# Optimization experiments

Hardware: AMD Instinct MI355X
Metric: run time of the kernel (lower is better)

## Reference

```python
import jax, jax.numpy as jnp
import numpy as np

L = 5          # num_layers
N = 50000      # nodes
E = 600000     # edges
D = 128        # num_features == hidden_units
G = 256        # graphs in batch
O = 10         # num_outputs
BN_EPS = 1e-5


def setup_inputs() -> dict:
    key = jax.random.key(0)
    ks = jax.random.split(key, 8)
    x = jax.random.normal(ks[0], (N, D), jnp.float32)
    edge_index = jax.random.randint(ks[1], (2, E), 0, N, jnp.int32)
    edge_attr = jax.random.randint(ks[2], (E, 3), 0, 8, jnp.int32)
    batch = jnp.sort(jax.random.randint(ks[3], (N,), 0, G, jnp.int32))
    s = 0.05
    return {
        "x": x,
        "edge_index": edge_index,
        "edge_attr": edge_attr,
        "batch": batch,
        "bond_emb": jax.random.normal(ks[4], (L, 3, 8, D), jnp.float32) * s,
        "conv_w1": jax.random.normal(ks[5], (L, D, D), jnp.float32) * s,
        "conv_b1": jnp.zeros((L, D), jnp.float32),
        "conv_bn_gamma": jnp.ones((L, D), jnp.float32),
        "conv_bn_beta": jnp.zeros((L, D), jnp.float32),
        "conv_bn_mean": jnp.zeros((L, D), jnp.float32),
        "conv_bn_var": jnp.ones((L, D), jnp.float32),
        "conv_w2": jax.random.normal(ks[6], (L, D, D), jnp.float32) * s,
        "conv_b2": jnp.zeros((L, D), jnp.float32),
        "bn_gamma": jnp.ones((L, D), jnp.float32),
        "bn_beta": jnp.zeros((L, D), jnp.float32),
        "bn_mean": jnp.zeros((L, D), jnp.float32),
        "bn_var": jnp.ones((L, D), jnp.float32),
        "fc_w": jax.random.normal(ks[7], (L + 1, D, O), jnp.float32) * s,
        "fc_b": jnp.zeros((L + 1, O), jnp.float32),
    }


def _bn_eval(h, gamma, beta, mean, var):
    return (h - mean) * jax.lax.rsqrt(var + BN_EPS) * gamma + beta


def reference(x, edge_index, edge_attr, batch, bond_emb,
              conv_w1, conv_b1, conv_bn_gamma, conv_bn_beta, conv_bn_mean, conv_bn_var,
              conv_w2, conv_b2, bn_gamma, bn_beta, bn_mean, bn_var, fc_w, fc_b):
    src, dst = edge_index[0], edge_index[1]  # x_j = x[src], aggregate at dst
    feat_ids = jnp.arange(3)
    outs = [x]
    for i in range(L):
        # BondEncoder: sum of per-feature embeddings -> [E, D]
        ea = bond_emb[i][feat_ids, edge_attr].sum(axis=1)
        # GINEConv (eps=0): msg = relu(x_j + edge_attr), scatter-add, nn(x + aggr)
        msg = jax.nn.relu(x[src] + ea)
        aggr = jax.ops.segment_sum(msg, dst, num_segments=N)
        h = x + aggr
        h = h @ conv_w1[i] + conv_b1[i]
        h = jax.nn.relu(_bn_eval(h, conv_bn_gamma[i], conv_bn_beta[i], conv_bn_mean[i], conv_bn_var[i]))
        h = h @ conv_w2[i] + conv_b2[i]
        x = jax.nn.relu(_bn_eval(h, bn_gamma[i], bn_beta[i], bn_mean[i], bn_var[i]))
        outs.append(x)
    # global mean pool per layer output, linear head, sum (dropout = identity in eval)
    counts = jax.ops.segment_sum(jnp.ones((N,), x.dtype), batch, num_segments=G)
    inv = 1.0 / jnp.maximum(counts, 1.0)
    out = jnp.zeros((G, O), x.dtype)
    for i, h in enumerate(outs):
        pooled = jax.ops.segment_sum(h, batch, num_segments=G) * inv[:, None]
        out = out + pooled @ fc_w[i] + fc_b[i]
    return out
```

## Files before the change

### kernel.cpp

```cpp
#include <hip/hip_runtime.h>

#define NN 50000
#define EE 600000
#define DD 128
#define GG 256
#define LL 5
#define OO 10
#define BN_EPS 1e-5f
#define CPAD 513
#define ESTRIDE 40
#define SENT (512u << 16)

#define B_SCAT  2344
#define B_CVT   3125
#define B_COMBO 1283
#define B_WT    160
#define B_INV   1
#define B_POOL0 391
#define B_STREAM (B_CVT + B_COMBO + B_WT + B_INV + B_POOL0)
#define B_PREP  (B_SCAT + B_STREAM)

typedef __attribute__((ext_vector_type(8))) short short8;
typedef __attribute__((ext_vector_type(16))) float float16;

__device__ __forceinline__ unsigned short f2b(float f) {
    unsigned u = __float_as_uint(f);
    unsigned r = u + 0x7FFFu + ((u >> 16) & 1u);
    return (unsigned short)(r >> 16);
}
__device__ __forceinline__ unsigned pk2(float lo, float hi) {
    return (unsigned)f2b(lo) | ((unsigned)f2b(hi) << 16);
}
__device__ __forceinline__ float blo(unsigned u) { return __uint_as_float(u << 16); }
__device__ __forceinline__ float bhi(unsigned u) { return __uint_as_float(u & 0xFFFF0000u); }

__launch_bounds__(256)
__global__ void prep(const float* __restrict__ x, const int* __restrict__ ei,
                     const int* __restrict__ eattr, const int* __restrict__ batch,
                     const float* __restrict__ bond,
                     const float* __restrict__ w1, const float* __restrict__ w2,
                     unsigned* __restrict__ xb4, unsigned short* __restrict__ combo,
                     short* __restrict__ wt, int* __restrict__ epos,
                     unsigned* __restrict__ e_info,
                     float* __restrict__ inv, float* __restrict__ pooled0) {
    const int bid = blockIdx.x, t = threadIdx.x;
    const int sc = (bid % 3 == 0) ? (bid / 3) : B_SCAT;
    if (sc < B_SCAT) {
        int e = sc * 256 + t;
        if (e < EE) {
            int dst = ei[EE + e];
            int slot = atomicAdd(&epos[dst], 1);
            if (slot < ESTRIDE) {
                unsigned cidx = (unsigned)eattr[e * 3 + 0] | ((unsigned)eattr[e * 3 + 1] << 3)
                              | ((unsigned)eattr[e * 3 + 2] << 6);
                e_info[dst * ESTRIDE + slot] = (unsigned)ei[e] | (cidx << 16);
            }
        }
        return;
    }
    int pr = (bid + 2) / 3; if (pr > B_SCAT) pr = B_SCAT;
    const int ob = bid - pr;
    if (ob < B_CVT) {
        int gid = ob * 256 + t;
        const float4* xp = (const float4*)(x + (size_t)gid * 8);
        float4 a = xp[0], b = xp[1];
        uint4 o;
        o.x = pk2(a.x, a.y); o.y = pk2(a.z, a.w);
        o.z = pk2(b.x, b.y); o.w = pk2(b.z, b.w);
        ((uint4*)xb4)[gid] = o;
    } else if (ob < B_CVT + B_COMBO) {
        int e = (ob - B_CVT) * 256 + t;
        if (e < LL * CPAD * DD) {
            int l = e / (CPAD * DD), rem = e - l * (CPAD * DD);
            int c = rem / DD, d = rem - c * DD;
            float s;
            if (c == 512) s = -1e30f;
            else {
                const float* b_ = bond + (size_t)l * 3 * 8 * DD;
                s = b_[(c & 7) * DD + d] + b_[(8 + ((c >> 3) & 7)) * DD + d]
                  + b_[(16 + (c >> 6)) * DD + d];
            }
            combo[e] = f2b(s);
        }
    } else if (ob < B_CVT + B_COMBO + B_WT) {
        __shared__ float tile[32][33];
        int b = ob - B_CVT - B_COMBO;
        int mat = b >> 4, tl = b & 15;
        int k0 = (tl >> 2) * 32, c0 = (tl & 3) * 32;
        const float* W = (mat < 5) ? (w1 + (size_t)mat * DD * DD)
                                   : (w2 + (size_t)(mat - 5) * DD * DD);
        int j = t & 31, q = t >> 5;
#pragma unroll
        for (int rr = 0; rr < 4; ++rr) {
            int row = q + rr * 8;
            tile[row][j] = W[(size_t)(k0 + row) * DD + c0 + j];
        }
        __syncthreads();
#pragma unroll
        for (int rr = 0; rr < 4; ++rr) {
            int cr = q + rr * 8;
            wt[(size_t)mat * DD * DD + (size_t)(c0 + cr) * DD + k0 + j] = (short)f2b(tile[j][cr]);
        }
    } else if (ob < B_CVT + B_COMBO + B_WT + B_INV) {
        __shared__ int sg[GG + 1];
        int g = t, lo = 0, hi = NN;
        while (lo < hi) { int m = (lo + hi) >> 1; if (batch[m] < g) lo = m + 1; else hi = m; }
        sg[g] = lo;
        if (g == 0) sg[GG] = NN;
        __syncthreads();
        inv[g] = 1.0f / fmaxf((float)(sg[g + 1] - sg[g]), 1.0f);
    } else {
        int b = ob - (B_CVT + B_COMBO + B_WT + B_INV);
        int n0 = b * 128;
        __shared__ int sb[128];
        __shared__ float part[4][DD];
        if (t < 128) { int row = n0 + t; sb[t] = (row < NN) ? batch[row] : -1; }
        ((float*)part)[t] = 0.f;
        ((float*)part)[t + 256] = 0.f;
        __syncthreads();
        int gmin = sb[0];
        int col = t & 127, rh = t >> 7;
        float pg[4] = {0.f, 0.f, 0.f, 0.f};
        for (int r = rh; r < 128; r += 2) {
            int s = sb[r];
            float v = (s >= 0) ? x[(size_t)(n0 + r) * DD + col] : 0.f;
            int dg = s - gmin;
#pragma unroll
            for (int jj = 0; jj < 4; ++jj) pg[jj] += (dg == jj) ? v : 0.f;
        }
#pragma unroll
        for (int jj = 0; jj < 4; ++jj)
            if (pg[jj] != 0.f) atomicAdd(&part[jj][col], pg[jj]);
        __syncthreads();
        for (int q2 = t; q2 < 4 * DD; q2 += 256) {
            int jj = q2 >> 7, c2 = q2 & 127;
            float v = part[jj][c2];
            if (v != 0.f && gmin + jj < GG) atomicAdd(&pooled0[(gmin + jj) * DD + c2], v);
        }
    }
}

__launch_bounds__(256)
__global__ void aggr_csr(const unsigned short* __restrict__ xin,
                         const int* __restrict__ epos,
                         const unsigned* __restrict__ e_info,
                         const unsigned short* __restrict__ combo,
                         unsigned short* __restrict__ hin) {
    int node = blockIdx.x * 4 + (threadIdx.x >> 6);
    int lane = threadIdx.x & 63;
    if (node >= NN) return;
    const int base = node * ESTRIDE;
    int deg = epos[node]; if (deg > ESTRIDE) deg = ESTRIDE;
    const int dend = base + deg;
    const int pe   = base + ((deg + 7) & ~7);
    const int eg   = lane >> 4;
    const int f    = (lane & 15) * 8;
    float acc[8];
#pragma unroll
    for (int i = 0; i < 8; ++i) acc[i] = 0.f;

    for (int p = base; p < pe; p += 8) {
        unsigned i0 = e_info[p + eg];
        unsigned i1 = e_info[p + 4 + eg];
        if (p + eg >= dend)     i0 = SENT;
        if (p + 4 + eg >= dend) i1 = SENT;
        uint4 xv0 = *(const uint4*)&xin[(size_t)(i0 & 0xFFFFu) * DD + f];
        uint4 cv0 = *(const uint4*)&combo[(size_t)(i0 >> 16) * DD + f];
        uint4 xv1 = *(const uint4*)&xin[(size_t)(i1 & 0xFFFFu) * DD + f];
        uint4 cv1 = *(const uint4*)&combo[(size_t)(i1 >> 16) * DD + f];
        acc[0] += fmaxf(blo(xv0.x) + blo(cv0.x), 0.f) + fmaxf(blo(xv1.x) + blo(cv1.x), 0.f);
        acc[1] += fmaxf(bhi(xv0.x) + bhi(cv0.x), 0.f) + fmaxf(bhi(xv1.x) + bhi(cv1.x), 0.f);
        acc[2] += fmaxf(blo(xv0.y) + blo(cv0.y), 0.f) + fmaxf(blo(xv1.y) + blo(cv1.y), 0.f);
        acc[3] += fmaxf(bhi(xv0.y) + bhi(cv0.y), 0.f) + fmaxf(bhi(xv1.y) + bhi(cv1.y), 0.f);
        acc[4] += fmaxf(blo(xv0.z) + blo(cv0.z), 0.f) + fmaxf(blo(xv1.z) + blo(cv1.z), 0.f);
        acc[5] += fmaxf(bhi(xv0.z) + bhi(cv0.z), 0.f) + fmaxf(bhi(xv1.z) + bhi(cv1.z), 0.f);
        acc[6] += fmaxf(blo(xv0.w) + blo(cv0.w), 0.f) + fmaxf(blo(xv1.w) + blo(cv1.w), 0.f);
        acc[7] += fmaxf(bhi(xv0.w) + bhi(cv0.w), 0.f) + fmaxf(bhi(xv1.w) + bhi(cv1.w), 0.f);
    }
#pragma unroll
    for (int i = 0; i < 8; ++i) {
        acc[i] += __shfl_xor(acc[i], 16, 64);
        acc[i] += __shfl_xor(acc[i], 32, 64);
    }
    if (lane < 16) {
        uint4 self = *(const uint4*)&xin[(size_t)node * DD + f];
        uint4 o;
        o.x = pk2(acc[0] + blo(self.x), acc[1] + bhi(self.x));
        o.y = pk2(acc[2] + blo(self.y), acc[3] + bhi(self.y));
        o.z = pk2(acc[4] + blo(self.z), acc[5] + bhi(self.z));
        o.w = pk2(acc[6] + blo(self.w), acc[7] + bhi(self.w));
        *(uint4*)&hin[(size_t)node * DD + f] = o;
    }
}

__launch_bounds__(256)
__global__ void conv_fused(const unsigned short* __restrict__ hin,
                           const short* __restrict__ Wt1, const short* __restrict__ Wt2,
                           const float* __restrict__ b1, const float* __restrict__ g1,
                           const float* __restrict__ be1, const float* __restrict__ m1,
                           const float* __restrict__ v1,
                           const float* __restrict__ b2, const float* __restrict__ g2,
                           const float* __restrict__ be2, const float* __restrict__ m2,
                           const float* __restrict__ v2,
                           const int* __restrict__ batch,
                           unsigned short* __restrict__ outb,
                           float* __restrict__ pool_slot) {
    __shared__ short As[64 * 136];
    __shared__ int sbg[64];
    const int tid  = threadIdx.x;
    const int lane = tid & 63;
    const int wave = tid >> 6;
    const int row0 = blockIdx.x * 64;

    const int col   = wave * 32 + (lane & 31);
    const int khalf = (lane >> 5) * 8;
    const int arow  = lane & 31;
    const int rbase = 4 * (lane >> 5);
    const int gmin  = batch[row0];

    short8 bf[8];
#pragma unroll
    for (int ch = 0; ch < 8; ++ch)
        bf[ch] = *(const short8*)&Wt1[col * DD + ch * 16 + khalf];

    const float sc1 = g1[col] * rsqrtf(v1[col] + BN_EPS);
    const float sh1 = fmaf(b1[col] - m1[col], sc1, be1[col]);
    const float sc2 = g2[col] * rsqrtf(v2[col] + BN_EPS);
    const float sh2 = fmaf(b2[col] - m2[col], sc2, be2[col]);

    if (tid < 64) {
        int row = row0 + tid;
        sbg[tid] = (row < NN) ? batch[row] - gmin : -1;
    }
    for (int i = tid; i < 1024; i += 256) {
        int r = i >> 4, c8 = (i & 15) * 8;
        int row = row0 + r;
        uint4 z = make_uint4(0, 0, 0, 0);
        if (row < NN) z = *(const uint4*)&hin[(size_t)row * DD + c8];
        *(uint4*)&As[r * 136 + c8] = z;
    }
    __syncthreads();

    float16 acc0 = {0.f,0.f,0.f,0.f,0.f,0.f,0.f,0.f,0.f,0.f,0.f,0.f,0.f,0.f,0.f,0.f};
    float16 acc1 = acc0;
#pragma unroll
    for (int ch = 0; ch < 8; ++ch) {
        short8 a0 = *(const short8*)&As[(arow     ) * 136 + ch * 16 + khalf];
        short8 a1 = *(const short8*)&As[(32 + arow) * 136 + ch * 16 + khalf];
        acc0 = __builtin_amdgcn_mfma_f32_32x32x16_bf16(a0, bf[ch], acc0, 0, 0, 0);
        acc1 = __builtin_amdgcn_mfma_f32_32x32x16_bf16(a1, bf[ch], acc1, 0, 0, 0);
    }

#pragma unroll
    for (int ch = 0; ch < 8; ++ch)
        bf[ch] = *(const short8*)&Wt2[col * DD + ch * 16 + khalf];

    __syncthreads();
#pragma unroll
    for (int r = 0; r < 16; ++r) {
        int rl = (r & 3) + 8 * (r >> 2) + rbase;
        As[rl * 136 + col]        = (short)f2b(fmaxf(fmaf(acc0[r], sc1, sh1), 0.f));
        As[(32 + rl) * 136 + col] = (short)f2b(fmaxf(fmaf(acc1[r], sc1, sh1), 0.f));
    }
    __syncthreads();

    acc0 = acc1 = float16{0.f,0.f,0.f,0.f,0.f,0.f,0.f,0.f,0.f,0.f,0.f,0.f,0.f,0.f,0.f,0.f};
#pragma unroll
    for (int ch = 0; ch < 8; ++ch) {
        short8 a0 = *(const short8*)&As[(arow     ) * 136 + ch * 16 + khalf];
        short8 a1 = *(const short8*)&As[(32 + arow) * 136 + ch * 16 + khalf];
        acc0 = __builtin_amdgcn_mfma_f32_32x32x16_bf16(a0, bf[ch], acc0, 0, 0, 0);
        acc1 = __builtin_amdgcn_mfma_f32_32x32x16_bf16(a1, bf[ch], acc1, 0, 0, 0);
    }

    float pg0 = 0.f, pg1 = 0.f, pg2 = 0.f, pg3 = 0.f;
#pragma unroll
    for (int r = 0; r < 16; ++r) {
        int rl  = (r & 3) + 8 * (r >> 2) + rbase;
        int row = row0 + rl;
        float v0 = fmaxf(fmaf(acc0[r], sc2, sh2), 0.f);
        float v1_ = fmaxf(fmaf(acc1[r], sc2, sh2), 0.f);
        if (row < NN)      outb[(size_t)row * DD + col]        = f2b(v0);
        if (row + 32 < NN) outb[(size_t)(row + 32) * DD + col] = f2b(v1_);
        int ga = sbg[rl], gb = sbg[rl + 32];
        pg0 += ((ga == 0) ? v0 : 0.f) + ((gb == 0) ? v1_ : 0.f);
        pg1 += ((ga == 1) ? v0 : 0.f) + ((gb == 1) ? v1_ : 0.f);
        pg2 += ((ga == 2) ? v0 : 0.f) + ((gb == 2) ? v1_ : 0.f);
        pg3 += ((ga == 3) ? v0 : 0.f) + ((gb == 3) ? v1_ : 0.f);
    }
    pg0 += __shfl_down(pg0, 32);
    pg1 += __shfl_down(pg1, 32);
    pg2 += __shfl_down(pg2, 32);
    pg3 += __shfl_down(pg3, 32);
    if (lane < 32) {
        if (pg0 != 0.f)                  atomicAdd(&pool_slot[(gmin    ) * DD + col], pg0);
        if (pg1 != 0.f && gmin + 1 < GG) atomicAdd(&pool_slot[(gmin + 1) * DD + col], pg1);
        if (pg2 != 0.f && gmin + 2 < GG) atomicAdd(&pool_slot[(gmin + 2) * DD + col], pg2);
        if (pg3 != 0.f && gmin + 3 < GG) atomicAdd(&pool_slot[(gmin + 3) * DD + col], pg3);
    }
}

__launch_bounds__(64)
__global__ void head(const float* __restrict__ pooled, const float* __restrict__ inv,
                     const float* __restrict__ fcw, const float* __restrict__ fcb,
                     float* __restrict__ out) {
    int g = blockIdx.x, t = threadIdx.x;
    __shared__ float part[LL + 1][OO];
    if (t < (LL + 1) * OO) {
        int l = t / OO, o2 = t - l * OO;
        const float* p = pooled + ((size_t)l * GG + g) * DD;
        const float* w = fcw + (size_t)l * DD * OO + o2;
        float s = 0.f;
        for (int d2 = 0; d2 < DD; ++d2) s = fmaf(p[d2], w[(size_t)d2 * OO], s);
        part[l][o2] = s;
    }
    __syncthreads();
    if (t < OO) {
        float sp = 0.f, sb2 = 0.f;
#pragma unroll
        for (int l = 0; l < LL + 1; ++l) { sp += part[l][t]; sb2 += fcb[l * OO + t]; }
        out[g * OO + t] = sp * inv[g] + sb2;
    }
}

extern "C" void kernel_launch(void* const* d_in, const int* in_sizes, int n_in,
                              void* d_out, int out_size, void* d_ws, size_t ws_size,
                              hipStream_t stream) {
    const float* x_in    = (const float*)d_in[0];
    const int*   ei      = (const int*)d_in[1];
    const int*   eattr   = (const int*)d_in[2];
    const int*   batch   = (const int*)d_in[3];
    const float* bond    = (const float*)d_in[4];
    const float* conv_w1 = (const float*)d_in[5];
    const float* conv_b1 = (const float*)d_in[6];
    const float* cbg     = (const float*)d_in[7];
    const float* cbb     = (const float*)d_in[8];
    const float* cbm     = (const float*)d_in[9];
    const float* cbv     = (const float*)d_in[10];
    const float* conv_w2 = (const float*)d_in[11];
    const float* conv_b2 = (const float*)d_in[12];
    const float* bg      = (const float*)d_in[13];
    const float* bb      = (const float*)d_in[14];
    const float* bm      = (const float*)d_in[15];
    const float* bv      = (const float*)d_in[16];
    const float* fcw     = (const float*)d_in[17];
    const float* fcb     = (const float*)d_in[18];
    float* out = (float*)d_out;

    char* base = (char*)d_ws;
    size_t o = 0;
    auto carve = [&](size_t bytes) { void* p = base + o; o += (bytes + 15) & ~(size_t)15; return p; };
    unsigned short* xbA    = (unsigned short*)carve((size_t)NN * DD * 2);
    unsigned short* xbB    = (unsigned short*)carve((size_t)NN * DD * 2);
    unsigned short* combo  = (unsigned short*)carve((size_t)LL * CPAD * DD * 2);
    short*          wt     = (short*)carve((size_t)10 * DD * DD * 2);
    float*          inv    = (float*)carve(GG * 4);
    const size_t ZBYTES = (size_t)NN * 4 + (size_t)(LL + 1) * GG * DD * 4;
    int*            epos   = (int*)carve(ZBYTES);
    float*          pooled = (float*)((char*)epos + (size_t)NN * 4);
    unsigned*       e_info = (unsigned*)carve((size_t)NN * ESTRIDE * 4);

    hipMemsetAsync(epos, 0, ZBYTES, stream);

    prep<<<B_PREP, 256, 0, stream>>>(x_in, ei, eattr, batch, bond, conv_w1, conv_w2,
                                     (unsigned*)xbA, combo, wt, epos, e_info, inv, pooled);

    const int conv_blocks = (NN + 63) / 64;
    const int aggr_blocks = (NN + 3) / 4;
    unsigned short* xin  = xbA;
    unsigned short* xout = xbB;
    for (int i = 0; i < LL; ++i) {
        aggr_csr<<<aggr_blocks, 256, 0, stream>>>(
            xin, epos, e_info, combo + (size_t)i * CPAD * DD, xout);
        conv_fused<<<conv_blocks, 256, 0, stream>>>(
            xout, wt + (size_t)i * DD * DD, wt + (size_t)(5 + i) * DD * DD,
            conv_b1 + (size_t)i * DD, cbg + (size_t)i * DD, cbb + (size_t)i * DD,
            cbm + (size_t)i * DD, cbv + (size_t)i * DD,
            conv_b2 + (size_t)i * DD, bg + (size_t)i * DD, bb + (size_t)i * DD,
            bm + (size_t)i * DD, bv + (size_t)i * DD,
            batch, xin, pooled + (size_t)(i + 1) * GG * DD);
    }
    head<<<GG, 64, 0, stream>>>(pooled, inv, fcw, fcb, out);
}
```

Before: 423.6 us.

## Fuse all stages into one persistent cooperative kernel with grid syncs

Replaces the sequence of separate launches (memset, prep, five aggregate/conv pairs, head) with a single cooperative persistent kernel. Blocks loop over virtual block indices, and grid.sync() separates the stages. The goal is to remove kernel launch gaps and the memset, at the cost of grid-wide barriers, reduced occupancy from a fixed persistent grid with a shared-memory union, and loss of the interleaved scatter ordering in prep. It falls back to the multi-kernel path when cooperative launch is unavailable.

Result: slower. 1.261 ms (+197.6%).

```diff
diff --git a/kernel.cpp b/kernel.cpp
--- a/kernel.cpp
+++ b/kernel.cpp
@@ -1,4 +1,7 @@
 #include <hip/hip_runtime.h>
+#include <hip/hip_cooperative_groups.h>
+
+namespace cg = cooperative_groups;
 
 #define NN 50000
 #define EE 600000
@@ -10,6 +13,7 @@
 #define CPAD 513
 #define ESTRIDE 40
 #define SENT (512u << 16)
+#define NT 256
 
 #define B_SCAT  2344
 #define B_CVT   3125
@@ -17,11 +21,25 @@
 #define B_WT    160
 #define B_INV   1
 #define B_POOL0 391
-#define B_STREAM (B_CVT + B_COMBO + B_WT + B_INV + B_POOL0)
-#define B_PREP  (B_SCAT + B_STREAM)
+#define B_PREP  (B_SCAT + B_CVT + B_COMBO + B_WT + B_INV + B_POOL0)
+
+#define AGGR_GRP ((NN + 3) / 4)
+#define CONV_TILES ((NN + 63) / 64)
+#define ZWORDS ((NN * 4 + (LL + 1) * GG * DD * 4) / 16)
 
 typedef __attribute__((ext_vector_type(8))) short short8;
 typedef __attribute__((ext_vector_type(16))) float float16;
+
+struct SmemT {
+    union {
+        short As[64 * 136];
+        float tile[32][33];
+        int   sg[GG + 1];
+        struct { int sb[128]; float part[4][DD]; } p0;
+        float hpart[LL + 1][OO];
+    } u;
+    int sbg[64];
+};
 
 __device__ __forceinline__ unsigned short f2b(float f) {
     unsigned u = __float_as_uint(f);
@@ -34,19 +52,18 @@
 __device__ __forceinline__ float blo(unsigned u) { return __uint_as_float(u << 16); }
 __device__ __forceinline__ float bhi(unsigned u) { return __uint_as_float(u & 0xFFFF0000u); }
 
-__launch_bounds__(256)
-__global__ void prep(const float* __restrict__ x, const int* __restrict__ ei,
-                     const int* __restrict__ eattr, const int* __restrict__ batch,
-                     const float* __restrict__ bond,
-                     const float* __restrict__ w1, const float* __restrict__ w2,
-                     unsigned* __restrict__ xb4, unsigned short* __restrict__ combo,
-                     short* __restrict__ wt, int* __restrict__ epos,
-                     unsigned* __restrict__ e_info,
-                     float* __restrict__ inv, float* __restrict__ pooled0) {
-    const int bid = blockIdx.x, t = threadIdx.x;
-    const int sc = (bid % 3 == 0) ? (bid / 3) : B_SCAT;
-    if (sc < B_SCAT) {
-        int e = sc * 256 + t;
+__device__ __forceinline__ void prep_vb(
+        int vb, int tid, SmemT& sm,
+        const float* __restrict__ x, const int* __restrict__ ei,
+        const int* __restrict__ eattr, const int* __restrict__ batch,
+        const float* __restrict__ bond,
+        const float* __restrict__ w1f, const float* __restrict__ w2f,
+        unsigned* __restrict__ xb4, unsigned short* __restrict__ combo,
+        short* __restrict__ wt, int* __restrict__ epos,
+        unsigned* __restrict__ e_info, float* __restrict__ inv,
+        float* __restrict__ pooled0) {
+    if (vb < B_SCAT) {
+        int e = vb * NT + tid;
         if (e < EE) {
             int dst = ei[EE + e];
             int slot = atomicAdd(&epos[dst], 1);
@@ -58,10 +75,9 @@
         }
         return;
     }
-    int pr = (bid + 2) / 3; if (pr > B_SCAT) pr = B_SCAT;
-    const int ob = bid - pr;
+    int ob = vb - B_SCAT;
     if (ob < B_CVT) {
-        int gid = ob * 256 + t;
+        int gid = ob * NT + tid;
         const float4* xp = (const float4*)(x + (size_t)gid * 8);
         float4 a = xp[0], b = xp[1];
         uint4 o;
@@ -69,7 +85,7 @@
         o.z = pk2(b.x, b.y); o.w = pk2(b.z, b.w);
         ((uint4*)xb4)[gid] = o;
     } else if (ob < B_CVT + B_COMBO) {
-        int e = (ob - B_CVT) * 256 + t;
+        int e = (ob - B_CVT) * NT + tid;
         if (e < LL * CPAD * DD) {
             int l = e / (CPAD * DD), rem = e - l * (CPAD * DD);
             int c = rem / DD, d = rem - c * DD;
@@ -83,46 +99,43 @@
             combo[e] = f2b(s);
         }
     } else if (ob < B_CVT + B_COMBO + B_WT) {
-        __shared__ float tile[32][33];
         int b = ob - B_CVT - B_COMBO;
         int mat = b >> 4, tl = b & 15;
         int k0 = (tl >> 2) * 32, c0 = (tl & 3) * 32;
-        const float* W = (mat < 5) ? (w1 + (size_t)mat * DD * DD)
-                                   : (w2 + (size_t)(mat - 5) * DD * DD);
-        int j = t & 31, q = t >> 5;
+        const float* W = (mat < 5) ? (w1f + (size_t)mat * DD * DD)
+                                   : (w2f + (size_t)(mat - 5) * DD * DD);
+        int j = tid & 31, q = tid >> 5;
 #pragma unroll
         for (int rr = 0; rr < 4; ++rr) {
             int row = q + rr * 8;
-            tile[row][j] = W[(size_t)(k0 + row) * DD + c0 + j];
+            sm.u.tile[row][j] = W[(size_t)(k0 + row) * DD + c0 + j];
         }
         __syncthreads();
 #pragma unroll
         for (int rr = 0; rr < 4; ++rr) {
             int cr = q + rr * 8;
-            wt[(size_t)mat * DD * DD + (size_t)(c0 + cr) * DD + k0 + j] = (short)f2b(tile[j][cr]);
+            wt[(size_t)mat * DD * DD + (size_t)(c0 + cr) * DD + k0 + j]
+                = (short)f2b(sm.u.tile[j][cr]);
         }
     } else if (ob < B_CVT + B_COMBO + B_WT + B_INV) {
-        __shared__ int sg[GG + 1];
-        int g = t, lo = 0, hi = NN;
+        int g = tid, lo = 0, hi = NN;
         while (lo < hi) { int m = (lo + hi) >> 1; if (batch[m] < g) lo = m + 1; else hi = m; }
-        sg[g] = lo;
-        if (g == 0) sg[GG] = NN;
+        sm.u.sg[g] = lo;
+        if (g == 0) sm.u.sg[GG] = NN;
         __syncthreads();
-        inv[g] = 1.0f / fmaxf((float)(sg[g + 1] - sg[g]), 1.0f);
+        inv[g] = 1.0f / fmaxf((float)(sm.u.sg[g + 1] - sm.u.sg[g]), 1.0f);
     } else {
         int b = ob - (B_CVT + B_COMBO + B_WT + B_INV);
         int n0 = b * 128;
-        __shared__ int sb[128];
-        __shared__ float part[4][DD];
-        if (t < 128) { int row = n0 + t; sb[t] = (row < NN) ? batch[row] : -1; }
-        ((float*)part)[t] = 0.f;
-        ((float*)part)[t + 256] = 0.f;
+        if (tid < 128) { int row = n0 + tid; sm.u.p0.sb[tid] = (row < NN) ? batch[row] : -1; }
+        ((float*)sm.u.p0.part)[tid] = 0.f;
+        ((float*)sm.u.p0.part)[tid + 256] = 0.f;
         __syncthreads();
-        int gmin = sb[0];
-        int col = t & 127, rh = t >> 7;
+        int gmin = sm.u.p0.sb[0];
+        int col = tid & 127, rh = tid >> 7;
         float pg[4] = {0.f, 0.f, 0.f, 0.f};
         for (int r = rh; r < 128; r += 2) {
-            int s = sb[r];
+            int s = sm.u.p0.sb[r];
             float v = (s >= 0) ? x[(size_t)(n0 + r) * DD + col] : 0.f;
             int dg = s - gmin;
 #pragma unroll
@@ -130,24 +143,23 @@
         }
 #pragma unroll
         for (int jj = 0; jj < 4; ++jj)
-            if (pg[jj] != 0.f) atomicAdd(&part[jj][col], pg[jj]);
+            if (pg[jj] != 0.f) atomicAdd(&sm.u.p0.part[jj][col], pg[jj]);
         __syncthreads();
-        for (int q2 = t; q2 < 4 * DD; q2 += 256) {
+        for (int q2 = tid; q2 < 4 * DD; q2 += NT) {
             int jj = q2 >> 7, c2 = q2 & 127;
-            float v = part[jj][c2];
+            float v = sm.u.p0.part[jj][c2];
             if (v != 0.f && gmin + jj < GG) atomicAdd(&pooled0[(gmin + jj) * DD + c2], v);
         }
     }
 }
 
-__launch_bounds__(256)
-__global__ void aggr_csr(const unsigned short* __restrict__ xin,
-                         const int* __restrict__ epos,
-                         const unsigned* __restrict__ e_info,
-                         const unsigned short* __restrict__ combo,
-                         unsigned short* __restrict__ hin) {
-    int node = blockIdx.x * 4 + (threadIdx.x >> 6);
-    int lane = threadIdx.x & 63;
+__device__ __forceinline__ void aggr_grp(
+        int grp, int tid,
+        const unsigned short* __restrict__ xb, const int* __restrict__ epos,
+        const unsigned* __restrict__ e_info, const unsigned short* __restrict__ cmb,
+        unsigned short* __restrict__ hin) {
+    int node = grp * 4 + (tid >> 6);
+    int lane = tid & 63;
     if (node >= NN) return;
     const int base = node * ESTRIDE;
     int deg = epos[node]; if (deg > ESTRIDE) deg = ESTRIDE;
@@ -158,16 +170,15 @@
     float acc[8];
 #pragma unroll
     for (int i = 0; i < 8; ++i) acc[i] = 0.f;
-
     for (int p = base; p < pe; p += 8) {
         unsigned i0 = e_info[p + eg];
         unsigned i1 = e_info[p + 4 + eg];
         if (p + eg >= dend)     i0 = SENT;
         if (p + 4 + eg >= dend) i1 = SENT;
-        uint4 xv0 = *(const uint4*)&xin[(size_t)(i0 & 0xFFFFu) * DD + f];
-        uint4 cv0 = *(const uint4*)&combo[(size_t)(i0 >> 16) * DD + f];
-        uint4 xv1 = *(const uint4*)&xin[(size_t)(i1 & 0xFFFFu) * DD + f];
-        uint4 cv1 = *(const uint4*)&combo[(size_t)(i1 >> 16) * DD + f];
+        uint4 xv0 = *(const uint4*)&xb[(size_t)(i0 & 0xFFFFu) * DD + f];
+        uint4 cv0 = *(const uint4*)&cmb[(size_t)(i0 >> 16) * DD + f];
+        uint4 xv1 = *(const uint4*)&xb[(size_t)(i1 & 0xFFFFu) * DD + f];
+        uint4 cv1 = *(const uint4*)&cmb[(size_t)(i1 >> 16) * DD + f];
         acc[0] += fmaxf(blo(xv0.x) + blo(cv0.x), 0.f) + fmaxf(blo(xv1.x) + blo(cv1.x), 0.f);
         acc[1] += fmaxf(bhi(xv0.x) + bhi(cv0.x), 0.f) + fmaxf(bhi(xv1.x) + bhi(cv1.x), 0.f);
         acc[2] += fmaxf(blo(xv0.y) + blo(cv0.y), 0.f) + fmaxf(blo(xv1.y) + blo(cv1.y), 0.f);
@@ -183,7 +194,7 @@
         acc[i] += __shfl_xor(acc[i], 32, 64);
     }
     if (lane < 16) {
-        uint4 self = *(const uint4*)&xin[(size_t)node * DD + f];
+        uint4 self = *(const uint4*)&xb[(size_t)node * DD + f];
         uint4 o;
         o.x = pk2(acc[0] + blo(self.x), acc[1] + bhi(self.x));
         o.y = pk2(acc[2] + blo(self.y), acc[3] + bhi(self.y));
@@ -193,51 +204,36 @@
     }
 }
 
-__launch_bounds__(256)
-__global__ void conv_fused(const unsigned short* __restrict__ hin,
-                           const short* __restrict__ Wt1, const short* __restrict__ Wt2,
-                           const float* __restrict__ b1, const float* __restrict__ g1,
-                           const float* __restrict__ be1, const float* __restrict__ m1,
-                           const float* __restrict__ v1,
-                           const float* __restrict__ b2, const float* __restrict__ g2,
-                           const float* __restrict__ be2, const float* __restrict__ m2,
-                           const float* __restrict__ v2,
-                           const int* __restrict__ batch,
-                           unsigned short* __restrict__ outb,
-                           float* __restrict__ pool_slot) {
-    __shared__ short As[64 * 136];
-    __shared__ int sbg[64];
-    const int tid  = threadIdx.x;
-    const int lane = tid & 63;
-    const int wave = tid >> 6;
-    const int row0 = blockIdx.x * 64;
-
+__device__ __forceinline__ void conv_tile(
+        int tl, int tid, SmemT& sm,
+        const unsigned short* __restrict__ hin,
+        const short* __restrict__ Wt1, const short* __restrict__ Wt2,
+        float sc1, float sh1, float sc2, float sh2,
+        const int* __restrict__ batch, unsigned short* __restrict__ outb,
+        float* __restrict__ pool_slot) {
+    const int lane  = tid & 63;
+    const int wave  = tid >> 6;
     const int col   = wave * 32 + (lane & 31);
     const int khalf = (lane >> 5) * 8;
     const int arow  = lane & 31;
     const int rbase = 4 * (lane >> 5);
+    const int row0  = tl * 64;
     const int gmin  = batch[row0];
 
     short8 bf[8];
 #pragma unroll
     for (int ch = 0; ch < 8; ++ch)
         bf[ch] = *(const short8*)&Wt1[col * DD + ch * 16 + khalf];
-
-    const float sc1 = g1[col] * rsqrtf(v1[col] + BN_EPS);
-    const float sh1 = fmaf(b1[col] - m1[col], sc1, be1[col]);
-    const float sc2 = g2[col] * rsqrtf(v2[col] + BN_EPS);
-    const float sh2 = fmaf(b2[col] - m2[col], sc2, be2[col]);
-
     if (tid < 64) {
         int row = row0 + tid;
-        sbg[tid] = (row < NN) ? batch[row] - gmin : -1;
-    }
-    for (int i = tid; i < 1024; i += 256) {
+        sm.sbg[tid] = (row < NN) ? batch[row] - gmin : -1;
+    }
+    for (int i = tid; i < 1024; i += NT) {
         int r = i >> 4, c8 = (i & 15) * 8;
         int row = row0 + r;
         uint4 z = make_uint4(0, 0, 0, 0);
         if (row < NN) z = *(const uint4*)&hin[(size_t)row * DD + c8];
-        *(uint4*)&As[r * 136 + c8] = z;
+        *(uint4*)&sm.u.As[r * 136 + c8] = z;
     }
     __syncthreads();
 
@@ -245,34 +241,30 @@
     float16 acc1 = acc0;
 #pragma unroll
     for (int ch = 0; ch < 8; ++ch) {
-        short8 a0 = *(const short8*)&As[(arow     ) * 136 + ch * 16 + khalf];
-        short8 a1 = *(const short8*)&As[(32 + arow) * 136 + ch * 16 + khalf];
+        short8 a0 = *(const short8*)&sm.u.As[(arow     ) * 136 + ch * 16 + khalf];
+        short8 a1 = *(const short8*)&sm.u.As[(32 + arow) * 136 + ch * 16 + khalf];
         acc0 = __builtin_amdgcn_mfma_f32_32x32x16_bf16(a0, bf[ch], acc0, 0, 0, 0);
         acc1 = __builtin_amdgcn_mfma_f32_32x32x16_bf16(a1, bf[ch], acc1, 0, 0, 0);
     }
-
 #pragma unroll
     for (int ch = 0; ch < 8; ++ch)
         bf[ch] = *(const short8*)&Wt2[col * DD + ch * 16 + khalf];
-
     __syncthreads();
 #pragma unroll
     for (int r = 0; r < 16; ++r) {
         int rl = (r & 3) + 8 * (r >> 2) + rbase;
-        As[rl * 136 + col]        = (short)f2b(fmaxf(fmaf(acc0[r], sc1, sh1), 0.f));
-        As[(32 + rl) * 136 + col] = (short)f2b(fmaxf(fmaf(acc1[r], sc1, sh1), 0.f));
+        sm.u.As[rl * 136 + col]        = (short)f2b(fmaxf(fmaf(acc0[r], sc1, sh1), 0.f));
+        sm.u.As[(32 + rl) * 136 + col] = (short)f2b(fmaxf(fmaf(acc1[r], sc1, sh1), 0.f));
     }
     __syncthreads();
-
     acc0 = acc1 = float16{0.f,0.f,0.f,0.f,0.f,0.f,0.f,0.f,0.f,0.f,0.f,0.f,0.f,0.f,0.f,0.f};
 #pragma unroll
     for (int ch = 0; ch < 8; ++ch) {
-        short8 a0 = *(const short8*)&As[(arow     ) * 136 + ch * 16 + khalf];
-        short8 a1 = *(const short8*)&As[(32 + arow) * 136 + ch * 16 + khalf];
+        short8 a0 = *(const short8*)&sm.u.As[(arow     ) * 136 + ch * 16 + khalf];
+        short8 a1 = *(const short8*)&sm.u.As[(32 + arow) * 136 + ch * 16 + khalf];
         acc0 = __builtin_amdgcn_mfma_f32_32x32x16_bf16(a0, bf[ch], acc0, 0, 0, 0);
         acc1 = __builtin_amdgcn_mfma_f32_32x32x16_bf16(a1, bf[ch], acc1, 0, 0, 0);
     }
-
     float pg0 = 0.f, pg1 = 0.f, pg2 = 0.f, pg3 = 0.f;
 #pragma unroll
     for (int r = 0; r < 16; ++r) {
@@ -282,7 +274,7 @@
         float v1_ = fmaxf(fmaf(acc1[r], sc2, sh2), 0.f);
         if (row < NN)      outb[(size_t)row * DD + col]        = f2b(v0);
         if (row + 32 < NN) outb[(size_t)(row + 32) * DD + col] = f2b(v1_);
-        int ga = sbg[rl], gb = sbg[rl + 32];
+        int ga = sm.sbg[rl], gb = sm.sbg[rl + 32];
         pg0 += ((ga == 0) ? v0 : 0.f) + ((gb == 0) ? v1_ : 0.f);
         pg1 += ((ga == 1) ? v0 : 0.f) + ((gb == 1) ? v1_ : 0.f);
         pg2 += ((ga == 2) ? v0 : 0.f) + ((gb == 2) ? v1_ : 0.f);
@@ -298,29 +290,125 @@
         if (pg2 != 0.f && gmin + 2 < GG) atomicAdd(&pool_slot[(gmin + 2) * DD + col], pg2);
         if (pg3 != 0.f && gmin + 3 < GG) atomicAdd(&pool_slot[(gmin + 3) * DD + col], pg3);
     }
-}
-
-__launch_bounds__(64)
-__global__ void head(const float* __restrict__ pooled, const float* __restrict__ inv,
-                     const float* __restrict__ fcw, const float* __restrict__ fcb,
-                     float* __restrict__ out) {
-    int g = blockIdx.x, t = threadIdx.x;
-    __shared__ float part[LL + 1][OO];
-    if (t < (LL + 1) * OO) {
-        int l = t / OO, o2 = t - l * OO;
+    __syncthreads();
+}
+
+__device__ __forceinline__ void head_blk(
+        int g, int tid, SmemT& sm,
+        const float* __restrict__ pooled, const float* __restrict__ inv,
+        const float* __restrict__ fcw, const float* __restrict__ fcb,
+        float* __restrict__ out) {
+    if (tid < (LL + 1) * OO) {
+        int l = tid / OO, o2 = tid - l * OO;
         const float* p = pooled + ((size_t)l * GG + g) * DD;
         const float* w = fcw + (size_t)l * DD * OO + o2;
         float s = 0.f;
         for (int d2 = 0; d2 < DD; ++d2) s = fmaf(p[d2], w[(size_t)d2 * OO], s);
-        part[l][o2] = s;
+        sm.u.hpart[l][o2] = s;
     }
     __syncthreads();
-    if (t < OO) {
+    if (tid < OO) {
         float sp = 0.f, sb2 = 0.f;
 #pragma unroll
-        for (int l = 0; l < LL + 1; ++l) { sp += part[l][t]; sb2 += fcb[l * OO + t]; }
-        out[g * OO + t] = sp * inv[g] + sb2;
-    }
+        for (int l = 0; l < LL + 1; ++l) { sp += sm.u.hpart[l][tid]; sb2 += fcb[l * OO + tid]; }
+        out[g * OO + tid] = sp * inv[g] + sb2;
+    }
+}
+
+__launch_bounds__(NT, 4)
+__global__ void gnn_all(const float* x, const int* ei, const int* eattr, const int* batch,
+                        const float* bond, const float* w1f, const float* w2f,
+                        const float* cb1, const float* cg1, const float* cbe1,
+                        const float* cm1, const float* cv1,
+                        const float* cb2, const float* cg2, const float* cbe2,
+                        const float* cm2, const float* cv2,
+                        const float* fcw, const float* fcb, float* out,
+                        unsigned short* xb, unsigned short* hin,
+                        unsigned short* combo, short* wt, float* inv,
+                        int* epos, float* pooled, unsigned* e_info) {
+    __shared__ SmemT sm;
+    cg::grid_group grid = cg::this_grid();
+    const int tid = threadIdx.x;
+    const int GB = gridDim.x;
+
+    {
+        uint4 z = make_uint4(0, 0, 0, 0);
+        uint4* zb = (uint4*)epos;
+        for (int i = blockIdx.x * NT + tid; i < ZWORDS; i += GB * NT) zb[i] = z;
+    }
+    grid.sync();
+
+    for (int vb = blockIdx.x; vb < B_PREP; vb += GB) {
+        prep_vb(vb, tid, sm, x, ei, eattr, batch, bond, w1f, w2f,
+                (unsigned*)xb, combo, wt, epos, e_info, inv, pooled);
+        __syncthreads();
+    }
+    grid.sync();
+
+    const int lane = tid & 63;
+    const int wave = tid >> 6;
+    const int col  = wave * 32 + (lane & 31);
+
+    for (int l = 0; l < LL; ++l) {
+        const unsigned short* cmb = combo + (size_t)l * CPAD * DD;
+        for (int grp = blockIdx.x; grp < AGGR_GRP; grp += GB)
+            aggr_grp(grp, tid, xb, epos, e_info, cmb, hin);
+        grid.sync();
+
+        const short* Wt1 = wt + (size_t)l * DD * DD;
+        const short* Wt2 = wt + (size_t)(5 + l) * DD * DD;
+        const float sc1 = cg1[l * DD + col] * rsqrtf(cv1[l * DD + col] + BN_EPS);
+        const float sh1 = fmaf(cb1[l * DD + col] - cm1[l * DD + col], sc1, cbe1[l * DD + col]);
+        const float sc2 = cg2[l * DD + col] * rsqrtf(cv2[l * DD + col] + BN_EPS);
+        const float sh2 = fmaf(cb2[l * DD + col] - cm2[l * DD + col], sc2, cbe2[l * DD + col]);
+        float* pool_slot = pooled + (size_t)(l + 1) * GG * DD;
+        for (int tl = blockIdx.x; tl < CONV_TILES; tl += GB)
+            conv_tile(tl, tid, sm, hin, Wt1, Wt2, sc1, sh1, sc2, sh2, batch, xb, pool_slot);
+        grid.sync();
+    }
+
+    if (blockIdx.x < GG)
+        head_blk(blockIdx.x, tid, sm, pooled, inv, fcw, fcb, out);
+}
+
+__launch_bounds__(NT)
+__global__ void prep_k(const float* x, const int* ei, const int* eattr, const int* batch,
+                       const float* bond, const float* w1f, const float* w2f,
+                       unsigned short* xb, unsigned short* combo, short* wt,
+                       int* epos, unsigned* e_info, float* inv, float* pooled0) {
+    __shared__ SmemT sm;
+    prep_vb(blockIdx.x, threadIdx.x, sm, x, ei, eattr, batch, bond, w1f, w2f,
+            (unsigned*)xb, combo, wt, epos, e_info, inv, pooled0);
+}
+
+__launch_bounds__(NT)
+__global__ void aggr_k(const unsigned short* xb, const int* epos, const unsigned* e_info,
+                       const unsigned short* cmb, unsigned short* hin) {
+    aggr_grp(blockIdx.x, threadIdx.x, xb, epos, e_info, cmb, hin);
+}
+
+__launch_bounds__(NT)
+__global__ void conv_k(const unsigned short* hin, const short* Wt1, const short* Wt2,
+                       const float* b1, const float* g1, const float* be1,
+                       const float* m1, const float* v1,
+                       const float* b2, const float* g2, const float* be2,
+                       const float* m2, const float* v2,
+                       const int* batch, unsigned short* outb, float* pool_slot) {
+    __shared__ SmemT sm;
+    const int tid = threadIdx.x;
+    const int col = (tid >> 6) * 32 + (tid & 31);
+    const float sc1 = g1[col] * rsqrtf(v1[col] + BN_EPS);
+    const float sh1 = fmaf(b1[col] - m1[col], sc1, be1[col]);
+    const float sc2 = g2[col] * rsqrtf(v2[col] + BN_EPS);
+    const float sh2 = fmaf(b2[col] - m2[col], sc2, be2[col]);
+    conv_tile(blockIdx.x, tid, sm, hin, Wt1, Wt2, sc1, sh1, sc2, sh2, batch, outb, pool_slot);
+}
+
+__launch_bounds__(64)
+__global__ void head_k(const float* pooled, const float* inv, const float* fcw,
+                       const float* fcb, float* out) {
+    __shared__ SmemT sm;
+    head_blk(blockIdx.x, threadIdx.x, sm, pooled, inv, fcw, fcb, out);
 }
 
 extern "C" void kernel_launch(void* const* d_in, const int* in_sizes, int n_in,
@@ -360,25 +448,47 @@
     float*          pooled = (float*)((char*)epos + (size_t)NN * 4);
     unsigned*       e_info = (unsigned*)carve((size_t)NN * ESTRIDE * 4);
 
-    hipMemsetAsync(epos, 0, ZBYTES, stream);
-
-    prep<<<B_PREP, 256, 0, stream>>>(x_in, ei, eattr, batch, bond, conv_w1, conv_w2,
-                                     (unsigned*)xbA, combo, wt, epos, e_info, inv, pooled);
-
-    const int conv_blocks = (NN + 63) / 64;
-    const int aggr_blocks = (NN + 3) / 4;
-    unsigned short* xin  = xbA;
-    unsigned short* xout = xbB;
-    for (int i = 0; i < LL; ++i) {
-        aggr_csr<<<aggr_blocks, 256, 0, stream>>>(
-            xin, epos, e_info, combo + (size_t)i * CPAD * DD, xout);
-        conv_fused<<<conv_blocks, 256, 0, stream>>>(
-            xout, wt + (size_t)i * DD * DD, wt + (size_t)(5 + i) * DD * DD,
-            conv_b1 + (size_t)i * DD, cbg + (size_t)i * DD, cbb + (size_t)i * DD,
-            cbm + (size_t)i * DD, cbv + (size_t)i * DD,
-            conv_b2 + (size_t)i * DD, bg + (size_t)i * DD, bb + (size_t)i * DD,
-            bm + (size_t)i * DD, bv + (size_t)i * DD,
-            batch, xin, pooled + (size_t)(i + 1) * GG * DD);
-    }
-    head<<<GG, 64, 0, stream>>>(pooled, inv, fcw, fcb, out);
-}
+    int dev = 0; hipGetDevice(&dev);
+    int coop = 0, ncu = 0, bpcu = 0;
+    hipDeviceGetAttribute(&coop, hipDeviceAttributeCooperativeLaunch, dev);
+    hipDeviceGetAttribute(&ncu, hipDeviceAttributeMultiprocessorCount, dev);
+    hipError_t occ = hipOccupancyMaxActiveBlocksPerMultiprocessor(
+        &bpcu, (const void*)gnn_all, NT, 0);
+    int grid = (occ == hipSuccess) ? bpcu * ncu : 0;
+    if (grid > 2048) grid = 2048;
+
+    bool done = false;
+    if (coop && grid >= GG) {
+        void* args[] = {
+            (void*)&x_in, (void*)&ei, (void*)&eattr, (void*)&batch, (void*)&bond,
+            (void*)&conv_w1, (void*)&conv_w2,
+            (void*)&conv_b1, (void*)&cbg, (void*)&cbb, (void*)&cbm, (void*)&cbv,
+            (void*)&conv_b2, (void*)&bg, (void*)&bb, (void*)&bm, (void*)&bv,
+            (void*)&fcw, (void*)&fcb, (void*)&out,
+            (void*)&xbA, (void*)&xbB, (void*)&combo, (void*)&wt, (void*)&inv,
+            (void*)&epos, (void*)&pooled, (void*)&e_info
+        };
+        hipError_t err = hipLaunchCooperativeKernel((const void*)gnn_all, dim3(grid),
+                                                    dim3(NT), args, 0, stream);
+        if (err == hipSuccess) done = true;
+        else (void)hipGetLastError();
+    }
+
+    if (!done) {
+        hipMemsetAsync(epos, 0, ZBYTES, stream);
+        prep_k<<<B_PREP, NT, 0, stream>>>(x_in, ei, eattr, batch, bond, conv_w1, conv_w2,
+                                          xbA, combo, wt, epos, e_info, inv, pooled);
+        for (int i = 0; i < LL; ++i) {
+            aggr_k<<<AGGR_GRP, NT, 0, stream>>>(
+                xbA, epos, e_info, combo + (size_t)i * CPAD * DD, xbB);
+            conv_k<<<CONV_TILES, NT, 0, stream>>>(
+                xbB, wt + (size_t)i * DD * DD, wt + (size_t)(5 + i) * DD * DD,
+                conv_b1 + (size_t)i * DD, cbg + (size_t)i * DD, cbb + (size_t)i * DD,
+                cbm + (size_t)i * DD, cbv + (size_t)i * DD,
+                conv_b2 + (size_t)i * DD, bg + (size_t)i * DD, bb + (size_t)i * DD,
+                bm + (size_t)i * DD, bv + (size_t)i * DD,
+                batch, xbA, pooled + (size_t)(i + 1) * GG * DD);
+        }
+        head_k<<<GG, 64, 0, stream>>>(pooled, inv, fcw, fcb, out);
+    }
+}
```
